# Performance work log

Hardware: AMD Instinct MI355X
Metric: run time of the kernel (lower is better)

## Reference

```python
import jax, jax.numpy as jnp
import numpy as np

B, T, H, L = 2048, 128, 48, 3  # batch, n_weights (= seq steps), hidden_dim, n_layers


def setup_inputs() -> dict:
    key = jax.random.key(0)
    ks = jax.random.split(key, 9)
    s = 0.05
    adj = jax.random.bernoulli(ks[0], 0.5, (B, T)).astype(jnp.float32)  # 0/1 adjacency entries
    eps = jax.random.normal(ks[1], (B, T), jnp.float32)  # standard-normal noise for rsample
    Wi = jax.random.normal(ks[2], (H, 1), jnp.float32) * s   # embed_input: Linear(1, H)
    bi = jnp.zeros((H,), jnp.float32)
    Wa = jax.random.normal(ks[3], (H, T), jnp.float32) * s   # embed_adj: Linear(n_weights, H)
    ba = jnp.zeros((H,), jnp.float32)
    Wp = jax.random.normal(ks[4], (1, H), jnp.float32) * s   # proj_mean: Linear(H, 1)
    bp = jnp.zeros((1,), jnp.float32)
    Wih = jax.random.normal(ks[5], (L, 4 * H, H), jnp.float32) * s  # LSTM input weights per layer
    Whh = jax.random.normal(ks[6], (L, 4 * H, H), jnp.float32) * s  # LSTM hidden weights per layer
    bih = jnp.zeros((L, 4 * H), jnp.float32)
    bhh = jnp.zeros((L, 4 * H), jnp.float32)
    h0 = 0.001 * jax.random.normal(ks[7], (L, H), jnp.float32)  # learned initial hidden state
    c0 = 0.001 * jax.random.normal(ks[8], (L, H), jnp.float32)  # learned initial cell state
    return dict(adj=adj, eps=eps, Wi=Wi, bi=bi, Wa=Wa, ba=ba, Wp=Wp, bp=bp,
                Wih=Wih, Whh=Whh, bih=bih, bhh=bhh, h0=h0, c0=c0)


def _lstm_cell(x, h, c, Wih_l, Whh_l, bih_l, bhh_l):
    # PyTorch LSTMCell math, gate order i, f, g, o
    gates = x @ Wih_l.T + bih_l + h @ Whh_l.T + bhh_l  # [B, 4H]
    i, f, g, o = jnp.split(gates, 4, axis=-1)
    c_new = jax.nn.sigmoid(f) * c + jax.nn.sigmoid(i) * jnp.tanh(g)
    h_new = jax.nn.sigmoid(o) * jnp.tanh(c_new)
    return h_new, c_new


def reference(adj, eps, Wi, bi, Wa, ba, Wp, bp, Wih, Whh, bih, bhh, h0, c0):
    n = adj.shape[0]
    # embed_adj(adj): constant across steps (the torch code recomputes it every step; same value)
    adj_emb = adj @ Wa.T + ba  # [B, H]
    h = jnp.broadcast_to(h0[:, None, :], (L, n, H))
    c = jnp.broadcast_to(c0[:, None, :], (L, n, H))
    inp0 = jnp.zeros((n, 1), adj.dtype)  # _init_input_param is a zeros parameter

    def step(carry, xs):
        h, c, inp = carry
        eps_t, adj_t = xs  # each [B]
        x = (inp @ Wi.T + bi) * adj_emb  # embed_input(inp) * embed_adj(adj), [B, H]
        hs, cs = [], []
        for l in range(L):  # 3 stacked LSTM layers, seq_len 1 per step
            x, c_l = _lstm_cell(x, h[l], c[l], Wih[l], Whh[l], bih[l], bhh[l])
            hs.append(x)
            cs.append(c_l)
        mean = x @ Wp.T + bp  # proj_mean, [B, 1]; std is fixed at 1
        # reparameterized sample from Normal(mean, 1), masked by adjacency column t
        sample = (mean[:, 0] + eps_t) * adj_t  # [B]
        return (jnp.stack(hs), jnp.stack(cs), sample[:, None]), sample

    _, samples = jax.lax.scan(step, (h, c, inp0), (eps.T, adj.T))
    return samples.T  # [B, n_weights]
```

## Files before the change

kernel.cpp:

```cpp
#include <hip/hip_runtime.h>
#include <hip/hip_bf16.h>


using bf16x8 = __attribute__((ext_vector_type(8))) __bf16;
using u16x8  = __attribute__((ext_vector_type(8))) unsigned short;
using f32x4  = __attribute__((ext_vector_type(4))) float;

__device__ __forceinline__ float fexp2(float x){ return __builtin_amdgcn_exp2f(x); }
__device__ __forceinline__ float frcp (float x){ return __builtin_amdgcn_rcpf(x); }
__device__ __forceinline__ float sigm (float x){ return frcp(1.f + fexp2(-1.44269504f*x)); }
__device__ __forceinline__ float tanha(float x){ return 1.f - 2.f*frcp(1.f + fexp2(2.88539008f*x)); }

__device__ __forceinline__ unsigned short f2bf(float x){
  unsigned u = __float_as_uint(x);
  return (unsigned short)((u + 0x7FFFu + ((u>>16)&1u)) >> 16);
}

__device__ __forceinline__ f32x4 mfma16(u16x8 a, u16x8 b, f32x4 c){
  return __builtin_amdgcn_mfma_f32_16x16x32_bf16(
      __builtin_bit_cast(bf16x8, a), __builtin_bit_cast(bf16x8, b), c, 0, 0, 0);
}

__device__ __forceinline__ unsigned cell2(
    const f32x4& ac0, const f32x4& ac1, const f32x4& ac2, const f32x4& ac3,
    bool lo, float& cv0, float& cv1)
{
  const float gi0 = lo ? ac0[0] : ac0[2], gi1 = lo ? ac0[1] : ac0[3];
  const float gf0 = lo ? ac1[0] : ac1[2], gf1 = lo ? ac1[1] : ac1[3];
  const float gg0 = lo ? ac2[0] : ac2[2], gg1 = lo ? ac2[1] : ac2[3];
  const float go0 = lo ? ac3[0] : ac3[2], go1 = lo ? ac3[1] : ac3[3];
  const float cn0 = sigm(gf0)*cv0 + sigm(gi0)*tanha(gg0);
  const float cn1 = sigm(gf1)*cv1 + sigm(gi1)*tanha(gg1);
  cv0 = cn0; cv1 = cn1;
  const float hv0 = sigm(go0)*tanha(cn0);
  const float hv1 = sigm(go1)*tanha(cn1);
  unsigned pk;
  asm("v_cvt_pk_bf16_f32 %0, %1, %2" : "=v"(pk) : "v"(hv0), "v"(hv1));
  return pk;
}

#define MM4(A, WK) \
  ac0 = mfma16(A, WK[0], ac0); ac1 = mfma16(A, WK[1], ac1); \
  ac2 = mfma16(A, WK[2], ac2); ac3 = mfma16(A, WK[3], ac3);

__global__ __launch_bounds__(192, 1) void lstm_fused(
    const float* __restrict__ adj, const float* __restrict__ eps,
    const float* __restrict__ Wi,  const float* __restrict__ bi,
    const float* __restrict__ Wa,  const float* __restrict__ ba,
    const float* __restrict__ Wp,  const float* __restrict__ bp,
    const float* __restrict__ Wih, const float* __restrict__ Whh,
    const float* __restrict__ bih, const float* __restrict__ bhh,
    const float* __restrict__ h0,  const float* __restrict__ c0,
    float* __restrict__ out)
{
  const int tid   = threadIdx.x;
  const int wv    = tid >> 6;
  const int lane  = tid & 63;
  const int c     = lane & 15;
  const int kg    = lane >> 4;
  const int j     = 16*wv + c;
  const int b0    = blockIdx.x * 8;
  const int bq    = 4*(kg & 1);
  const int bbase = bq + 2*(kg >> 1);
  const bool lo   = (kg < 2);

  __shared__ __align__(16) unsigned short hbuf[3][8][104];
  __shared__ __align__(16) float adjT[128][8];
  __shared__ __align__(16) float epsT[128][8];
  __shared__ __align__(16) float outb[128][8];

  u16x8 wf1[3][4], wf2[3][4];
  u16x8 wf0[2][4], wfx[2][4];
  u16x8 wpf[2];
  float biasr1[4], biasr2[4], biasr0[4];
#pragma unroll
  for (int kk = 0; kk < 3; ++kk) {
    const int k0 = 32*kk + 8*kg;
#pragma unroll
    for (int g = 0; g < 4; ++g) {
      const int n = 48*g + j;
#pragma unroll
      for (int l = 1; l < 3; ++l) {
        const float* src = (k0 < 48) ? (Wih + ((l*192 + n)*48 + k0))
                                     : (Whh + ((l*192 + n)*48 + (k0 - 48)));
        float4 p0 = *reinterpret_cast<const float4*>(src);
        float4 p1 = *reinterpret_cast<const float4*>(src + 4);
        u16x8 f;
        f[0]=f2bf(p0.x); f[1]=f2bf(p0.y); f[2]=f2bf(p0.z); f[3]=f2bf(p0.w);
        f[4]=f2bf(p1.x); f[5]=f2bf(p1.y); f[6]=f2bf(p1.z); f[7]=f2bf(p1.w);
        if (l == 1) wf1[kk][g] = f; else wf2[kk][g] = f;
      }
    }
  }
#pragma unroll
  for (int kk = 0; kk < 2; ++kk) {
    const int k0 = 32*kk + 8*kg;
#pragma unroll
    for (int g = 0; g < 4; ++g) {
      const int n = 48*g + j;
      u16x8 fh = {0,0,0,0,0,0,0,0}, fx = fh;
      if (k0 < 48) {
        const float* sh = Whh + (n*48 + k0);
        const float* sx = Wih + (n*48 + k0);
        float4 p0 = *reinterpret_cast<const float4*>(sh);
        float4 p1 = *reinterpret_cast<const float4*>(sh + 4);
        fh[0]=f2bf(p0.x); fh[1]=f2bf(p0.y); fh[2]=f2bf(p0.z); fh[3]=f2bf(p0.w);
        fh[4]=f2bf(p1.x); fh[5]=f2bf(p1.y); fh[6]=f2bf(p1.z); fh[7]=f2bf(p1.w);
        p0 = *reinterpret_cast<const float4*>(sx);
        p1 = *reinterpret_cast<const float4*>(sx + 4);
        fx[0]=f2bf(p0.x); fx[1]=f2bf(p0.y); fx[2]=f2bf(p0.z); fx[3]=f2bf(p0.w);
        fx[4]=f2bf(p1.x); fx[5]=f2bf(p1.y); fx[6]=f2bf(p1.z); fx[7]=f2bf(p1.w);
      }
      wf0[kk][g] = fh; wfx[kk][g] = fx;
    }
    u16x8 fp = {0,0,0,0,0,0,0,0};
#pragma unroll
    for (int e = 0; e < 8; ++e) {
      const int k = k0 + e;
      if (k < 48) fp[e] = f2bf(Wp[k]);
    }
    wpf[kk] = fp;
  }
#pragma unroll
  for (int g = 0; g < 4; ++g) {
    const int n = 48*g + j;
    biasr0[g] = bih[        n] + bhh[        n];
    biasr1[g] = bih[192   + n] + bhh[192   + n];
    biasr2[g] = bih[2*192 + n] + bhh[2*192 + n];
  }

  for (int i = tid; i < 256; i += 192) {
    const int b = i >> 5, q = i & 31;
    const float4 va = reinterpret_cast<const float4*>(adj + (size_t)(b0+b)*128)[q];
    adjT[4*q+0][b]=va.x; adjT[4*q+1][b]=va.y; adjT[4*q+2][b]=va.z; adjT[4*q+3][b]=va.w;
    const float4 ve = reinterpret_cast<const float4*>(eps + (size_t)(b0+b)*128)[q];
    epsT[4*q+0][b]=ve.x; epsT[4*q+1][b]=ve.y; epsT[4*q+2][b]=ve.z; epsT[4*q+3][b]=ve.w;
  }
  const float bp0 = bp[0];
  __syncthreads();

  for (int cid = tid; cid < 384; cid += 192) {
    const int b = cid & 7, jj = cid >> 3;
    float s = ba[jj];
    const float* wr = Wa + jj*128;
    for (int t2 = 0; t2 < 128; ++t2) s += adjT[t2][b] * wr[t2];
    hbuf[0][b][jj] = f2bf(Wi[jj] * s);
    hbuf[1][b][jj] = f2bf(bi[jj] * s);
  }
  for (int cid = tid; cid < 384; cid += 192) {
    const int l = cid / 128, r2 = cid % 128, b = r2 >> 4, jj = 48 + (r2 & 15);
    hbuf[l][b][jj] = 0;
  }
  __syncthreads();

  f32x4 uu[4], vb0[4];
  {
    const f32x4 z4 = {0.f,0.f,0.f,0.f};
    const unsigned short* rp = &hbuf[0][c & 7][0];
    u16x8 A0 = *reinterpret_cast<const u16x8*>(rp + 8*kg);
    u16x8 A1 = *reinterpret_cast<const u16x8*>(rp + 32 + 8*kg);
#pragma unroll
    for (int g = 0; g < 4; ++g)
      uu[g] = mfma16(A1, wfx[1][g], mfma16(A0, wfx[0][g], z4));
    rp = &hbuf[1][c & 7][0];
    A0 = *reinterpret_cast<const u16x8*>(rp + 8*kg);
    A1 = *reinterpret_cast<const u16x8*>(rp + 32 + 8*kg);
#pragma unroll
    for (int g = 0; g < 4; ++g) {
      f32x4 v = mfma16(A1, wfx[1][g], mfma16(A0, wfx[0][g], z4));
      const f32x4 bsp = {biasr0[g], biasr0[g], biasr0[g], biasr0[g]};
      vb0[g] = v + bsp;
    }
  }
  __syncthreads();

  for (int cid = tid; cid < 1152; cid += 192) {
    const int l = cid / 384, r2 = cid % 384, b = r2 & 7, jj = r2 >> 3;
    hbuf[l][b][jj] = f2bf(h0[l*48 + jj]);
  }
  float cc00, cc01, cc10, cc11, cc20, cc21;
  cc00 = cc01 = c0[       j];
  cc10 = cc11 = c0[48   + j];
  cc20 = cc21 = c0[2*48 + j];
  __syncthreads();

  f32x4 g0, g1, g2, g3;
  {
    const unsigned short* rp = &hbuf[0][c & 7][0];
    const u16x8 A0 = *reinterpret_cast<const u16x8*>(rp + 8*kg);
    const u16x8 A1 = *reinterpret_cast<const u16x8*>(rp + 32 + 8*kg);
    g0 = vb0[0]; g1 = vb0[1]; g2 = vb0[2]; g3 = vb0[3];
    g0 = mfma16(A0, wf0[0][0], g0); g1 = mfma16(A0, wf0[0][1], g1);
    g2 = mfma16(A0, wf0[0][2], g2); g3 = mfma16(A0, wf0[0][3], g3);
    g0 = mfma16(A1, wf0[1][0], g0); g1 = mfma16(A1, wf0[1][1], g1);
    g2 = mfma16(A1, wf0[1][2], g2); g3 = mfma16(A1, wf0[1][3], g3);
  }

  const f32x4 bp4 = {bp0, bp0, bp0, bp0};
  f32x4 sampv = {0.f,0.f,0.f,0.f};

  for (int t = 0; t < 128; ++t) {
    if (t) {
      const u16x8 mh0 = *reinterpret_cast<const u16x8*>(&hbuf[2][c & 7][8*kg]);
      const u16x8 mh1 = *reinterpret_cast<const u16x8*>(&hbuf[2][c & 7][32 + 8*kg]);
      const f32x4 ev = *reinterpret_cast<const f32x4*>(&epsT[t-1][bq]);
      const f32x4 av = *reinterpret_cast<const f32x4*>(&adjT[t-1][bq]);
      f32x4 mz = {0.f,0.f,0.f,0.f};
      mz = mfma16(mh0, wpf[0], mz);
      mz = mfma16(mh1, wpf[1], mz);
      sampv = (mz + bp4 + ev) * av;
      if (tid == 0 || tid == 16)
        *reinterpret_cast<f32x4*>(&outb[t-1][bq]) = sampv;
    }
    g0 += sampv*uu[0]; g1 += sampv*uu[1]; g2 += sampv*uu[2]; g3 += sampv*uu[3];
    {
      const unsigned pk = cell2(g0, g1, g2, g3, lo, cc00, cc01);
      hbuf[0][bbase    ][j] = (unsigned short)pk;
      hbuf[0][bbase + 1][j] = (unsigned short)(pk >> 16);
    }
    u16x8 a11 = {0,0,0,0,0,0,0,0}, a12;
    if (kg >= 2) a11 = *reinterpret_cast<const u16x8*>(&hbuf[1][c & 7][8*kg - 16]);
    a12 = *reinterpret_cast<const u16x8*>(&hbuf[1][c & 7][16 + 8*kg]);
    __syncthreads();
    {
      const unsigned short* rp = &hbuf[0][c & 7][0];
      const u16x8 a10 = *reinterpret_cast<const u16x8*>(rp + 8*kg);
      if (kg < 2) a11 = *reinterpret_cast<const u16x8*>(rp + 32 + 8*kg);
      f32x4 ac0 = {biasr1[0], biasr1[0], biasr1[0], biasr1[0]};
      f32x4 ac1 = {biasr1[1], biasr1[1], biasr1[1], biasr1[1]};
      f32x4 ac2 = {biasr1[2], biasr1[2], biasr1[2], biasr1[2]};
      f32x4 ac3 = {biasr1[3], biasr1[3], biasr1[3], biasr1[3]};
      MM4(a12, wf1[2]);
      MM4(a10, wf1[0]);
      MM4(a11, wf1[1]);
      const unsigned pk = cell2(ac0, ac1, ac2, ac3, lo, cc10, cc11);
      hbuf[1][bbase    ][j] = (unsigned short)pk;
      hbuf[1][bbase + 1][j] = (unsigned short)(pk >> 16);
    }
    u16x8 a21 = {0,0,0,0,0,0,0,0}, a22;
    if (kg >= 2) a21 = *reinterpret_cast<const u16x8*>(&hbuf[2][c & 7][8*kg - 16]);
    a22 = *reinterpret_cast<const u16x8*>(&hbuf[2][c & 7][16 + 8*kg]);
    __syncthreads();
    {
      const unsigned short* rp = &hbuf[1][c & 7][0];
      const u16x8 a20 = *reinterpret_cast<const u16x8*>(rp + 8*kg);
      if (kg < 2) a21 = *reinterpret_cast<const u16x8*>(rp + 32 + 8*kg);
      const unsigned short* rp0 = &hbuf[0][c & 7][0];
      const u16x8 a00 = *reinterpret_cast<const u16x8*>(rp0 + 8*kg);
      const u16x8 a01 = *reinterpret_cast<const u16x8*>(rp0 + 32 + 8*kg);
      f32x4 ac0 = {biasr2[0], biasr2[0], biasr2[0], biasr2[0]};
      f32x4 ac1 = {biasr2[1], biasr2[1], biasr2[1], biasr2[1]};
      f32x4 ac2 = {biasr2[2], biasr2[2], biasr2[2], biasr2[2]};
      f32x4 ac3 = {biasr2[3], biasr2[3], biasr2[3], biasr2[3]};
      MM4(a22, wf2[2]);
      MM4(a20, wf2[0]);
      MM4(a21, wf2[1]);
      const unsigned pk = cell2(ac0, ac1, ac2, ac3, lo, cc20, cc21);
      hbuf[2][bbase    ][j] = (unsigned short)pk;
      hbuf[2][bbase + 1][j] = (unsigned short)(pk >> 16);
      g0 = vb0[0]; g1 = vb0[1]; g2 = vb0[2]; g3 = vb0[3];
      g0 = mfma16(a00, wf0[0][0], g0); g1 = mfma16(a00, wf0[0][1], g1);
      g2 = mfma16(a00, wf0[0][2], g2); g3 = mfma16(a00, wf0[0][3], g3);
      g0 = mfma16(a01, wf0[1][0], g0); g1 = mfma16(a01, wf0[1][1], g1);
      g2 = mfma16(a01, wf0[1][2], g2); g3 = mfma16(a01, wf0[1][3], g3);
    }
    __syncthreads();
  }
  {
    const u16x8 mh0 = *reinterpret_cast<const u16x8*>(&hbuf[2][c & 7][8*kg]);
    const u16x8 mh1 = *reinterpret_cast<const u16x8*>(&hbuf[2][c & 7][32 + 8*kg]);
    const f32x4 ev = *reinterpret_cast<const f32x4*>(&epsT[127][bq]);
    const f32x4 av = *reinterpret_cast<const f32x4*>(&adjT[127][bq]);
    f32x4 mz = {0.f,0.f,0.f,0.f};
    mz = mfma16(mh0, wpf[0], mz);
    mz = mfma16(mh1, wpf[1], mz);
    const f32x4 sv = (mz + bp4 + ev) * av;
    if (tid == 0 || tid == 16)
      *reinterpret_cast<f32x4*>(&outb[127][bq]) = sv;
  }
  __syncthreads();
  for (int i = tid; i < 1024; i += 192) {
    const int b = i >> 7, tt = i & 127;
    out[(size_t)(b0 + b)*128 + tt] = outb[tt][b];
  }
}

extern "C" void kernel_launch(void* const* d_in, const int* in_sizes, int n_in,
                              void* d_out, int out_size, void* d_ws, size_t ws_size,
                              hipStream_t stream) {
  const float* adj = (const float*)d_in[0];
  const float* eps = (const float*)d_in[1];
  const float* Wi  = (const float*)d_in[2];
  const float* bi  = (const float*)d_in[3];
  const float* Wa  = (const float*)d_in[4];
  const float* ba  = (const float*)d_in[5];
  const float* Wp  = (const float*)d_in[6];
  const float* bp  = (const float*)d_in[7];
  const float* Wih = (const float*)d_in[8];
  const float* Whh = (const float*)d_in[9];
  const float* bih = (const float*)d_in[10];
  const float* bhh = (const float*)d_in[11];
  const float* h0  = (const float*)d_in[12];
  const float* c0  = (const float*)d_in[13];

  lstm_fused<<<dim3(2048/8), dim3(192), 0, stream>>>(
      adj, eps, Wi, bi, Wa, ba, Wp, bp, Wih, Whh, bih, bhh, h0, c0, (float*)d_out);
}
```

Baseline: 150.5 us.

## Halve batch rows per block to double grid and occupancy

Each block now handles 4 batch rows instead of 8, so the grid doubles to 512 blocks and launch bounds allow 2 blocks per CU. Each lane now computes one LSTM cell element instead of two. The MFMA work per block stays the same size, so half the MMA rows are wasted on duplicated batch rows. The aim is to spread the latency-bound recurrence over more CUs and let two blocks per CU overlap their barrier stalls, at the cost of more redundant weight loading and higher register pressure.

```diff
diff --git a/kernel.cpp b/kernel.cpp
--- a/kernel.cpp
+++ b/kernel.cpp
@@ -21,29 +21,17 @@
       __builtin_bit_cast(bf16x8, a), __builtin_bit_cast(bf16x8, b), c, 0, 0, 0);
 }
 
-__device__ __forceinline__ unsigned cell2(
-    const f32x4& ac0, const f32x4& ac1, const f32x4& ac2, const f32x4& ac3,
-    bool lo, float& cv0, float& cv1)
-{
-  const float gi0 = lo ? ac0[0] : ac0[2], gi1 = lo ? ac0[1] : ac0[3];
-  const float gf0 = lo ? ac1[0] : ac1[2], gf1 = lo ? ac1[1] : ac1[3];
-  const float gg0 = lo ? ac2[0] : ac2[2], gg1 = lo ? ac2[1] : ac2[3];
-  const float go0 = lo ? ac3[0] : ac3[2], go1 = lo ? ac3[1] : ac3[3];
-  const float cn0 = sigm(gf0)*cv0 + sigm(gi0)*tanha(gg0);
-  const float cn1 = sigm(gf1)*cv1 + sigm(gi1)*tanha(gg1);
-  cv0 = cn0; cv1 = cn1;
-  const float hv0 = sigm(go0)*tanha(cn0);
-  const float hv1 = sigm(go1)*tanha(cn1);
-  unsigned pk;
-  asm("v_cvt_pk_bf16_f32 %0, %1, %2" : "=v"(pk) : "v"(hv0), "v"(hv1));
-  return pk;
+__device__ __forceinline__ float sel4(const f32x4& a, int kg){
+  const float e01 = (kg & 1) ? a[1] : a[0];
+  const float e23 = (kg & 1) ? a[3] : a[2];
+  return (kg & 2) ? e23 : e01;
 }
 
 #define MM4(A, WK) \
   ac0 = mfma16(A, WK[0], ac0); ac1 = mfma16(A, WK[1], ac1); \
   ac2 = mfma16(A, WK[2], ac2); ac3 = mfma16(A, WK[3], ac3);
 
-__global__ __launch_bounds__(192, 1) void lstm_fused(
+__global__ __launch_bounds__(192, 2) void lstm_fused(
     const float* __restrict__ adj, const float* __restrict__ eps,
     const float* __restrict__ Wi,  const float* __restrict__ bi,
     const float* __restrict__ Wa,  const float* __restrict__ ba,
@@ -53,26 +41,24 @@
     const float* __restrict__ h0,  const float* __restrict__ c0,
     float* __restrict__ out)
 {
-  const int tid   = threadIdx.x;
-  const int wv    = tid >> 6;
-  const int lane  = tid & 63;
-  const int c     = lane & 15;
-  const int kg    = lane >> 4;
-  const int j     = 16*wv + c;
-  const int b0    = blockIdx.x * 8;
-  const int bq    = 4*(kg & 1);
-  const int bbase = bq + 2*(kg >> 1);
-  const bool lo   = (kg < 2);
-
-  __shared__ __align__(16) unsigned short hbuf[3][8][104];
-  __shared__ __align__(16) float adjT[128][8];
-  __shared__ __align__(16) float epsT[128][8];
-  __shared__ __align__(16) float outb[128][8];
+  const int tid  = threadIdx.x;
+  const int wv   = tid >> 6;
+  const int lane = tid & 63;
+  const int c    = lane & 15;
+  const int kg   = lane >> 4;
+  const int j    = 16*wv + c;
+  const int b0   = blockIdx.x * 4;
+  const int cr   = c & 3;
+
+  __shared__ __align__(16) unsigned short hbuf[3][4][104];
+  __shared__ __align__(16) float adjT[128][4];
+  __shared__ __align__(16) float epsT[128][4];
+  __shared__ __align__(16) float outb[128][4];
 
   u16x8 wf1[3][4], wf2[3][4];
   u16x8 wf0[2][4], wfx[2][4];
   u16x8 wpf[2];
-  float biasr1[4], biasr2[4], biasr0[4];
+  float biasr0[4], biasr1[4], biasr2[4];
 #pragma unroll
   for (int kk = 0; kk < 3; ++kk) {
     const int k0 = 32*kk + 8*kg;
@@ -129,8 +115,8 @@
     biasr2[g] = bih[2*192 + n] + bhh[2*192 + n];
   }
 
-  for (int i = tid; i < 256; i += 192) {
-    const int b = i >> 5, q = i & 31;
+  if (tid < 128) {
+    const int b = tid >> 5, q = tid & 31;
     const float4 va = reinterpret_cast<const float4*>(adj + (size_t)(b0+b)*128)[q];
     adjT[4*q+0][b]=va.x; adjT[4*q+1][b]=va.y; adjT[4*q+2][b]=va.z; adjT[4*q+3][b]=va.w;
     const float4 ve = reinterpret_cast<const float4*>(eps + (size_t)(b0+b)*128)[q];
@@ -139,57 +125,55 @@
   const float bp0 = bp[0];
   __syncthreads();
 
-  for (int cid = tid; cid < 384; cid += 192) {
-    const int b = cid & 7, jj = cid >> 3;
+  {
+    const int b = tid & 3, jj = tid >> 2;
     float s = ba[jj];
     const float* wr = Wa + jj*128;
     for (int t2 = 0; t2 < 128; ++t2) s += adjT[t2][b] * wr[t2];
     hbuf[0][b][jj] = f2bf(Wi[jj] * s);
     hbuf[1][b][jj] = f2bf(bi[jj] * s);
-  }
-  for (int cid = tid; cid < 384; cid += 192) {
-    const int l = cid / 128, r2 = cid % 128, b = r2 >> 4, jj = 48 + (r2 & 15);
-    hbuf[l][b][jj] = 0;
-  }
-  __syncthreads();
-
-  f32x4 uu[4], vb0[4];
+    hbuf[wv][lane >> 4][48 + (lane & 15)] = 0;
+  }
+  __syncthreads();
+
+  float u_k[4], vb_k[4];
   {
     const f32x4 z4 = {0.f,0.f,0.f,0.f};
-    const unsigned short* rp = &hbuf[0][c & 7][0];
+    const unsigned short* rp = &hbuf[0][cr][0];
     u16x8 A0 = *reinterpret_cast<const u16x8*>(rp + 8*kg);
     u16x8 A1 = *reinterpret_cast<const u16x8*>(rp + 32 + 8*kg);
 #pragma unroll
-    for (int g = 0; g < 4; ++g)
-      uu[g] = mfma16(A1, wfx[1][g], mfma16(A0, wfx[0][g], z4));
-    rp = &hbuf[1][c & 7][0];
+    for (int g = 0; g < 4; ++g) {
+      f32x4 u = mfma16(A1, wfx[1][g], mfma16(A0, wfx[0][g], z4));
+      u_k[g] = sel4(u, kg);
+    }
+    rp = &hbuf[1][cr][0];
     A0 = *reinterpret_cast<const u16x8*>(rp + 8*kg);
     A1 = *reinterpret_cast<const u16x8*>(rp + 32 + 8*kg);
 #pragma unroll
     for (int g = 0; g < 4; ++g) {
       f32x4 v = mfma16(A1, wfx[1][g], mfma16(A0, wfx[0][g], z4));
-      const f32x4 bsp = {biasr0[g], biasr0[g], biasr0[g], biasr0[g]};
-      vb0[g] = v + bsp;
-    }
-  }
-  __syncthreads();
-
-  for (int cid = tid; cid < 1152; cid += 192) {
-    const int l = cid / 384, r2 = cid % 384, b = r2 & 7, jj = r2 >> 3;
+      vb_k[g] = sel4(v, kg) + biasr0[g];
+    }
+  }
+  __syncthreads();
+
+  for (int cid = tid; cid < 576; cid += 192) {
+    const int l = cid / 192, r2 = cid % 192, b = r2 & 3, jj = r2 >> 2;
     hbuf[l][b][jj] = f2bf(h0[l*48 + jj]);
   }
-  float cc00, cc01, cc10, cc11, cc20, cc21;
-  cc00 = cc01 = c0[       j];
-  cc10 = cc11 = c0[48   + j];
-  cc20 = cc21 = c0[2*48 + j];
+  float cv0 = c0[j], cv1 = c0[48 + j], cv2 = c0[2*48 + j];
   __syncthreads();
 
   f32x4 g0, g1, g2, g3;
   {
-    const unsigned short* rp = &hbuf[0][c & 7][0];
+    const unsigned short* rp = &hbuf[0][cr][0];
     const u16x8 A0 = *reinterpret_cast<const u16x8*>(rp + 8*kg);
     const u16x8 A1 = *reinterpret_cast<const u16x8*>(rp + 32 + 8*kg);
-    g0 = vb0[0]; g1 = vb0[1]; g2 = vb0[2]; g3 = vb0[3];
+    g0 = (f32x4){vb_k[0], vb_k[0], vb_k[0], vb_k[0]};
+    g1 = (f32x4){vb_k[1], vb_k[1], vb_k[1], vb_k[1]};
+    g2 = (f32x4){vb_k[2], vb_k[2], vb_k[2], vb_k[2]};
+    g3 = (f32x4){vb_k[3], vb_k[3], vb_k[3], vb_k[3]};
     g0 = mfma16(A0, wf0[0][0], g0); g1 = mfma16(A0, wf0[0][1], g1);
     g2 = mfma16(A0, wf0[0][2], g2); g3 = mfma16(A0, wf0[0][3], g3);
     g0 = mfma16(A1, wf0[1][0], g0); g1 = mfma16(A1, wf0[1][1], g1);
@@ -197,33 +181,36 @@
   }
 
   const f32x4 bp4 = {bp0, bp0, bp0, bp0};
-  f32x4 sampv = {0.f,0.f,0.f,0.f};
+  f32x4 avR = {0.f,0.f,0.f,0.f}, evR = avR;
 
   for (int t = 0; t < 128; ++t) {
+    float s_kg = 0.f;
     if (t) {
-      const u16x8 mh0 = *reinterpret_cast<const u16x8*>(&hbuf[2][c & 7][8*kg]);
-      const u16x8 mh1 = *reinterpret_cast<const u16x8*>(&hbuf[2][c & 7][32 + 8*kg]);
-      const f32x4 ev = *reinterpret_cast<const f32x4*>(&epsT[t-1][bq]);
-      const f32x4 av = *reinterpret_cast<const f32x4*>(&adjT[t-1][bq]);
+      const u16x8 mh0 = *reinterpret_cast<const u16x8*>(&hbuf[2][cr][8*kg]);
+      const u16x8 mh1 = *reinterpret_cast<const u16x8*>(&hbuf[2][cr][32 + 8*kg]);
       f32x4 mz = {0.f,0.f,0.f,0.f};
       mz = mfma16(mh0, wpf[0], mz);
       mz = mfma16(mh1, wpf[1], mz);
-      sampv = (mz + bp4 + ev) * av;
-      if (tid == 0 || tid == 16)
-        *reinterpret_cast<f32x4*>(&outb[t-1][bq]) = sampv;
-    }
-    g0 += sampv*uu[0]; g1 += sampv*uu[1]; g2 += sampv*uu[2]; g3 += sampv*uu[3];
+      const f32x4 sampv = (mz + bp4 + evR) * avR;
+      if (tid == 0)
+        *reinterpret_cast<f32x4*>(&outb[t-1][0]) = sampv;
+      s_kg = sel4(sampv, kg);
+    }
     {
-      const unsigned pk = cell2(g0, g1, g2, g3, lo, cc00, cc01);
-      hbuf[0][bbase    ][j] = (unsigned short)pk;
-      hbuf[0][bbase + 1][j] = (unsigned short)(pk >> 16);
+      const float gi = sel4(g0, kg) + s_kg*u_k[0];
+      const float gf = sel4(g1, kg) + s_kg*u_k[1];
+      const float gg = sel4(g2, kg) + s_kg*u_k[2];
+      const float go = sel4(g3, kg) + s_kg*u_k[3];
+      const float cn = sigm(gf)*cv0 + sigm(gi)*tanha(gg);
+      cv0 = cn;
+      hbuf[0][kg][j] = f2bf(sigm(go)*tanha(cn));
     }
     u16x8 a11 = {0,0,0,0,0,0,0,0}, a12;
-    if (kg >= 2) a11 = *reinterpret_cast<const u16x8*>(&hbuf[1][c & 7][8*kg - 16]);
-    a12 = *reinterpret_cast<const u16x8*>(&hbuf[1][c & 7][16 + 8*kg]);
+    if (kg >= 2) a11 = *reinterpret_cast<const u16x8*>(&hbuf[1][cr][8*kg - 16]);
+    a12 = *reinterpret_cast<const u16x8*>(&hbuf[1][cr][16 + 8*kg]);
     __syncthreads();
     {
-      const unsigned short* rp = &hbuf[0][c & 7][0];
+      const unsigned short* rp = &hbuf[0][cr][0];
       const u16x8 a10 = *reinterpret_cast<const u16x8*>(rp + 8*kg);
       if (kg < 2) a11 = *reinterpret_cast<const u16x8*>(rp + 32 + 8*kg);
       f32x4 ac0 = {biasr1[0], biasr1[0], biasr1[0], biasr1[0]};
@@ -233,21 +220,25 @@
       MM4(a12, wf1[2]);
       MM4(a10, wf1[0]);
       MM4(a11, wf1[1]);
-      const unsigned pk = cell2(ac0, ac1, ac2, ac3, lo, cc10, cc11);
-      hbuf[1][bbase    ][j] = (unsigned short)pk;
-      hbuf[1][bbase + 1][j] = (unsigned short)(pk >> 16);
+      const float gi = sel4(ac0, kg), gf = sel4(ac1, kg);
+      const float gg = sel4(ac2, kg), go = sel4(ac3, kg);
+      const float cn = sigm(gf)*cv1 + sigm(gi)*tanha(gg);
+      cv1 = cn;
+      hbuf[1][kg][j] = f2bf(sigm(go)*tanha(cn));
     }
     u16x8 a21 = {0,0,0,0,0,0,0,0}, a22;
-    if (kg >= 2) a21 = *reinterpret_cast<const u16x8*>(&hbuf[2][c & 7][8*kg - 16]);
-    a22 = *reinterpret_cast<const u16x8*>(&hbuf[2][c & 7][16 + 8*kg]);
+    if (kg >= 2) a21 = *reinterpret_cast<const u16x8*>(&hbuf[2][cr][8*kg - 16]);
+    a22 = *reinterpret_cast<const u16x8*>(&hbuf[2][cr][16 + 8*kg]);
     __syncthreads();
     {
-      const unsigned short* rp = &hbuf[1][c & 7][0];
+      const unsigned short* rp = &hbuf[1][cr][0];
       const u16x8 a20 = *reinterpret_cast<const u16x8*>(rp + 8*kg);
       if (kg < 2) a21 = *reinterpret_cast<const u16x8*>(rp + 32 + 8*kg);
-      const unsigned short* rp0 = &hbuf[0][c & 7][0];
+      const unsigned short* rp0 = &hbuf[0][cr][0];
       const u16x8 a00 = *reinterpret_cast<const u16x8*>(rp0 + 8*kg);
       const u16x8 a01 = *reinterpret_cast<const u16x8*>(rp0 + 32 + 8*kg);
+      avR = *reinterpret_cast<const f32x4*>(&adjT[t][0]);
+      evR = *reinterpret_cast<const f32x4*>(&epsT[t][0]);
       f32x4 ac0 = {biasr2[0], biasr2[0], biasr2[0], biasr2[0]};
       f32x4 ac1 = {biasr2[1], biasr2[1], biasr2[1], biasr2[1]};
       f32x4 ac2 = {biasr2[2], biasr2[2], biasr2[2], biasr2[2]};
@@ -255,10 +246,15 @@
       MM4(a22, wf2[2]);
       MM4(a20, wf2[0]);
       MM4(a21, wf2[1]);
-      const unsigned pk = cell2(ac0, ac1, ac2, ac3, lo, cc20, cc21);
-      hbuf[2][bbase    ][j] = (unsigned short)pk;
-      hbuf[2][bbase + 1][j] = (unsigned short)(pk >> 16);
-      g0 = vb0[0]; g1 = vb0[1]; g2 = vb0[2]; g3 = vb0[3];
+      const float gi = sel4(ac0, kg), gf = sel4(ac1, kg);
+      const float gg = sel4(ac2, kg), go = sel4(ac3, kg);
+      const float cn = sigm(gf)*cv2 + sigm(gi)*tanha(gg);
+      cv2 = cn;
+      hbuf[2][kg][j] = f2bf(sigm(go)*tanha(cn));
+      g0 = (f32x4){vb_k[0], vb_k[0], vb_k[0], vb_k[0]};
+      g1 = (f32x4){vb_k[1], vb_k[1], vb_k[1], vb_k[1]};
+      g2 = (f32x4){vb_k[2], vb_k[2], vb_k[2], vb_k[2]};
+      g3 = (f32x4){vb_k[3], vb_k[3], vb_k[3], vb_k[3]};
       g0 = mfma16(a00, wf0[0][0], g0); g1 = mfma16(a00, wf0[0][1], g1);
       g2 = mfma16(a00, wf0[0][2], g2); g3 = mfma16(a00, wf0[0][3], g3);
       g0 = mfma16(a01, wf0[1][0], g0); g1 = mfma16(a01, wf0[1][1], g1);
@@ -267,19 +263,17 @@
     __syncthreads();
   }
   {
-    const u16x8 mh0 = *reinterpret_cast<const u16x8*>(&hbuf[2][c & 7][8*kg]);
-    const u16x8 mh1 = *reinterpret_cast<const u16x8*>(&hbuf[2][c & 7][32 + 8*kg]);
-    const f32x4 ev = *reinterpret_cast<const f32x4*>(&epsT[127][bq]);
-    const f32x4 av = *reinterpret_cast<const f32x4*>(&adjT[127][bq]);
+    const u16x8 mh0 = *reinterpret_cast<const u16x8*>(&hbuf[2][cr][8*kg]);
+    const u16x8 mh1 = *reinterpret_cast<const u16x8*>(&hbuf[2][cr][32 + 8*kg]);
     f32x4 mz = {0.f,0.f,0.f,0.f};
     mz = mfma16(mh0, wpf[0], mz);
     mz = mfma16(mh1, wpf[1], mz);
-    const f32x4 sv = (mz + bp4 + ev) * av;
-    if (tid == 0 || tid == 16)
-      *reinterpret_cast<f32x4*>(&outb[127][bq]) = sv;
-  }
-  __syncthreads();
-  for (int i = tid; i < 1024; i += 192) {
+    const f32x4 sv = (mz + bp4 + evR) * avR;
+    if (tid == 0)
+      *reinterpret_cast<f32x4*>(&outb[127][0]) = sv;
+  }
+  __syncthreads();
+  for (int i = tid; i < 512; i += 192) {
     const int b = i >> 7, tt = i & 127;
     out[(size_t)(b0 + b)*128 + tt] = outb[tt][b];
   }
@@ -303,6 +297,6 @@
   const float* h0  = (const float*)d_in[12];
   const float* c0  = (const float*)d_in[13];
 
-  lstm_fused<<<dim3(2048/8), dim3(192), 0, stream>>>(
+  lstm_fused<<<dim3(2048/4), dim3(192), 0, stream>>>(
       adj, eps, Wi, bi, Wa, ba, Wp, bp, Wih, Whh, bih, bhh, h0, c0, (float*)d_out);
 }
```

New measurement: 180.3 us. 19.8% more time.

## Restructure LSTM step: fewer transcendentals, hoisted MFMAs before barriers, split projection chains

Applied to the files above, without the earlier changes.

Rewrites the LSTM cell to use algebraically combined exp2 terms and a single reciprocal for the cell update and one for the output, instead of separate sigmoid/tanh reciprocals. Issues the MFMAs that depend only on already-available hidden state (the recurrent-h slice) before each barrier so they overlap the synchronization wait. Splits the projection MFMA into two independent accumulators, prefetches eps/adj a step early, and handles feedback per selected element rather than full vectors. The combined-exp formulation risks overflow/inf for large gate magnitudes and changes rounding slightly.

```diff
diff --git a/kernel.cpp b/kernel.cpp
--- a/kernel.cpp
+++ b/kernel.cpp
@@ -8,8 +8,6 @@
 
 __device__ __forceinline__ float fexp2(float x){ return __builtin_amdgcn_exp2f(x); }
 __device__ __forceinline__ float frcp (float x){ return __builtin_amdgcn_rcpf(x); }
-__device__ __forceinline__ float sigm (float x){ return frcp(1.f + fexp2(-1.44269504f*x)); }
-__device__ __forceinline__ float tanha(float x){ return 1.f - 2.f*frcp(1.f + fexp2(2.88539008f*x)); }
 
 __device__ __forceinline__ unsigned short f2bf(float x){
   unsigned u = __float_as_uint(x);
@@ -21,22 +19,20 @@
       __builtin_bit_cast(bf16x8, a), __builtin_bit_cast(bf16x8, b), c, 0, 0, 0);
 }
 
-__device__ __forceinline__ unsigned cell2(
-    const f32x4& ac0, const f32x4& ac1, const f32x4& ac2, const f32x4& ac3,
-    bool lo, float& cv0, float& cv1)
-{
-  const float gi0 = lo ? ac0[0] : ac0[2], gi1 = lo ? ac0[1] : ac0[3];
-  const float gf0 = lo ? ac1[0] : ac1[2], gf1 = lo ? ac1[1] : ac1[3];
-  const float gg0 = lo ? ac2[0] : ac2[2], gg1 = lo ? ac2[1] : ac2[3];
-  const float go0 = lo ? ac3[0] : ac3[2], go1 = lo ? ac3[1] : ac3[3];
-  const float cn0 = sigm(gf0)*cv0 + sigm(gi0)*tanha(gg0);
-  const float cn1 = sigm(gf1)*cv1 + sigm(gi1)*tanha(gg1);
-  cv0 = cn0; cv1 = cn1;
-  const float hv0 = sigm(go0)*tanha(cn0);
-  const float hv1 = sigm(go1)*tanha(cn1);
-  unsigned pk;
-  asm("v_cvt_pk_bf16_f32 %0, %1, %2" : "=v"(pk) : "v"(hv0), "v"(hv1));
-  return pk;
+__device__ __forceinline__ float selA(const f32x4& a, bool lo){ return lo ? a[0] : a[2]; }
+__device__ __forceinline__ float selB(const f32x4& a, bool lo){ return lo ? a[1] : a[3]; }
+
+__device__ __forceinline__ float cell_h(float gi, float gf, float gg, float go, float& cv){
+  const float A = fexp2(-1.44269504f*gf);
+  const float B = fexp2(-1.44269504f*gi);
+  const float G = fexp2(-2.88539008f*gg);
+  const float pBG = (1.f+B)*(1.f+G);
+  const float nc  = cv*pBG + (1.f+A)*(1.f-G);
+  const float cn  = nc * frcp((1.f+A)*pBG);
+  cv = cn;
+  const float O = fexp2(-1.44269504f*go);
+  const float C = fexp2(-2.88539008f*cn);
+  return (1.f-C) * frcp((1.f+O)*(1.f+C));
 }
 
 #define MM4(A, WK) \
@@ -63,6 +59,7 @@
   const int bq    = 4*(kg & 1);
   const int bbase = bq + 2*(kg >> 1);
   const bool lo   = (kg < 2);
+  const int cr    = c & 7;
 
   __shared__ __align__(16) unsigned short hbuf[3][8][104];
   __shared__ __align__(16) float adjT[128][8];
@@ -72,7 +69,7 @@
   u16x8 wf1[3][4], wf2[3][4];
   u16x8 wf0[2][4], wfx[2][4];
   u16x8 wpf[2];
-  float biasr1[4], biasr2[4], biasr0[4];
+  float biasr0[4], biasr1[4], biasr2[4];
 #pragma unroll
   for (int kk = 0; kk < 3; ++kk) {
     const int k0 = 32*kk + 8*kg;
@@ -153,23 +150,25 @@
   }
   __syncthreads();
 
-  f32x4 uu[4], vb0[4];
+  float uA[4], uB[4], vbA[4], vbB[4];
   {
     const f32x4 z4 = {0.f,0.f,0.f,0.f};
-    const unsigned short* rp = &hbuf[0][c & 7][0];
+    const unsigned short* rp = &hbuf[0][cr][0];
     u16x8 A0 = *reinterpret_cast<const u16x8*>(rp + 8*kg);
     u16x8 A1 = *reinterpret_cast<const u16x8*>(rp + 32 + 8*kg);
 #pragma unroll
-    for (int g = 0; g < 4; ++g)
-      uu[g] = mfma16(A1, wfx[1][g], mfma16(A0, wfx[0][g], z4));
-    rp = &hbuf[1][c & 7][0];
+    for (int g = 0; g < 4; ++g) {
+      f32x4 u = mfma16(A1, wfx[1][g], mfma16(A0, wfx[0][g], z4));
+      uA[g] = selA(u, lo); uB[g] = selB(u, lo);
+    }
+    rp = &hbuf[1][cr][0];
     A0 = *reinterpret_cast<const u16x8*>(rp + 8*kg);
     A1 = *reinterpret_cast<const u16x8*>(rp + 32 + 8*kg);
 #pragma unroll
     for (int g = 0; g < 4; ++g) {
       f32x4 v = mfma16(A1, wfx[1][g], mfma16(A0, wfx[0][g], z4));
-      const f32x4 bsp = {biasr0[g], biasr0[g], biasr0[g], biasr0[g]};
-      vb0[g] = v + bsp;
+      vbA[g] = selA(v, lo) + biasr0[g];
+      vbB[g] = selB(v, lo) + biasr0[g];
     }
   }
   __syncthreads();
@@ -178,18 +177,21 @@
     const int l = cid / 384, r2 = cid % 384, b = r2 & 7, jj = r2 >> 3;
     hbuf[l][b][jj] = f2bf(h0[l*48 + jj]);
   }
-  float cc00, cc01, cc10, cc11, cc20, cc21;
-  cc00 = cc01 = c0[       j];
-  cc10 = cc11 = c0[48   + j];
-  cc20 = cc21 = c0[2*48 + j];
+  float cc0A, cc0B, cc1A, cc1B, cc2A, cc2B;
+  cc0A = cc0B = c0[       j];
+  cc1A = cc1B = c0[48   + j];
+  cc2A = cc2B = c0[2*48 + j];
   __syncthreads();
 
   f32x4 g0, g1, g2, g3;
   {
-    const unsigned short* rp = &hbuf[0][c & 7][0];
+    const unsigned short* rp = &hbuf[0][cr][0];
     const u16x8 A0 = *reinterpret_cast<const u16x8*>(rp + 8*kg);
     const u16x8 A1 = *reinterpret_cast<const u16x8*>(rp + 32 + 8*kg);
-    g0 = vb0[0]; g1 = vb0[1]; g2 = vb0[2]; g3 = vb0[3];
+    g0 = (f32x4){vbA[0], vbB[0], vbA[0], vbB[0]};
+    g1 = (f32x4){vbA[1], vbB[1], vbA[1], vbB[1]};
+    g2 = (f32x4){vbA[2], vbB[2], vbA[2], vbB[2]};
+    g3 = (f32x4){vbA[3], vbB[3], vbA[3], vbB[3]};
     g0 = mfma16(A0, wf0[0][0], g0); g1 = mfma16(A0, wf0[0][1], g1);
     g2 = mfma16(A0, wf0[0][2], g2); g3 = mfma16(A0, wf0[0][3], g3);
     g0 = mfma16(A1, wf0[1][0], g0); g1 = mfma16(A1, wf0[1][1], g1);
@@ -197,68 +199,85 @@
   }
 
   const f32x4 bp4 = {bp0, bp0, bp0, bp0};
-  f32x4 sampv = {0.f,0.f,0.f,0.f};
+  f32x4 avR = {0.f,0.f,0.f,0.f}, evR = avR;
 
   for (int t = 0; t < 128; ++t) {
+    float sA = 0.f, sB = 0.f;
     if (t) {
-      const u16x8 mh0 = *reinterpret_cast<const u16x8*>(&hbuf[2][c & 7][8*kg]);
-      const u16x8 mh1 = *reinterpret_cast<const u16x8*>(&hbuf[2][c & 7][32 + 8*kg]);
-      const f32x4 ev = *reinterpret_cast<const f32x4*>(&epsT[t-1][bq]);
-      const f32x4 av = *reinterpret_cast<const f32x4*>(&adjT[t-1][bq]);
-      f32x4 mz = {0.f,0.f,0.f,0.f};
-      mz = mfma16(mh0, wpf[0], mz);
-      mz = mfma16(mh1, wpf[1], mz);
-      sampv = (mz + bp4 + ev) * av;
+      const u16x8 mh0 = *reinterpret_cast<const u16x8*>(&hbuf[2][cr][8*kg]);
+      const u16x8 mh1 = *reinterpret_cast<const u16x8*>(&hbuf[2][cr][32 + 8*kg]);
+      f32x4 mz0 = {0.f,0.f,0.f,0.f}, mz1 = mz0;
+      mz0 = mfma16(mh0, wpf[0], mz0);
+      mz1 = mfma16(mh1, wpf[1], mz1);
+      const f32x4 sampv = (mz0 + mz1 + bp4 + evR) * avR;
       if (tid == 0 || tid == 16)
         *reinterpret_cast<f32x4*>(&outb[t-1][bq]) = sampv;
-    }
-    g0 += sampv*uu[0]; g1 += sampv*uu[1]; g2 += sampv*uu[2]; g3 += sampv*uu[3];
+      sA = selA(sampv, lo); sB = selB(sampv, lo);
+    }
+    u16x8 a11 = {0,0,0,0,0,0,0,0}, a12;
+    if (kg >= 2) a11 = *reinterpret_cast<const u16x8*>(&hbuf[1][cr][8*kg - 16]);
+    a12 = *reinterpret_cast<const u16x8*>(&hbuf[1][cr][16 + 8*kg]);
     {
-      const unsigned pk = cell2(g0, g1, g2, g3, lo, cc00, cc01);
+      const float hA = cell_h(selA(g0,lo)+sA*uA[0], selA(g1,lo)+sA*uA[1],
+                              selA(g2,lo)+sA*uA[2], selA(g3,lo)+sA*uA[3], cc0A);
+      const float hB = cell_h(selB(g0,lo)+sB*uB[0], selB(g1,lo)+sB*uB[1],
+                              selB(g2,lo)+sB*uB[2], selB(g3,lo)+sB*uB[3], cc0B);
+      unsigned pk;
+      asm("v_cvt_pk_bf16_f32 %0, %1, %2" : "=v"(pk) : "v"(hA), "v"(hB));
       hbuf[0][bbase    ][j] = (unsigned short)pk;
       hbuf[0][bbase + 1][j] = (unsigned short)(pk >> 16);
     }
-    u16x8 a11 = {0,0,0,0,0,0,0,0}, a12;
-    if (kg >= 2) a11 = *reinterpret_cast<const u16x8*>(&hbuf[1][c & 7][8*kg - 16]);
-    a12 = *reinterpret_cast<const u16x8*>(&hbuf[1][c & 7][16 + 8*kg]);
+    f32x4 ac0 = {biasr1[0], biasr1[0], biasr1[0], biasr1[0]};
+    f32x4 ac1 = {biasr1[1], biasr1[1], biasr1[1], biasr1[1]};
+    f32x4 ac2 = {biasr1[2], biasr1[2], biasr1[2], biasr1[2]};
+    f32x4 ac3 = {biasr1[3], biasr1[3], biasr1[3], biasr1[3]};
+    MM4(a12, wf1[2]);
     __syncthreads();
     {
-      const unsigned short* rp = &hbuf[0][c & 7][0];
+      const unsigned short* rp = &hbuf[0][cr][0];
       const u16x8 a10 = *reinterpret_cast<const u16x8*>(rp + 8*kg);
       if (kg < 2) a11 = *reinterpret_cast<const u16x8*>(rp + 32 + 8*kg);
-      f32x4 ac0 = {biasr1[0], biasr1[0], biasr1[0], biasr1[0]};
-      f32x4 ac1 = {biasr1[1], biasr1[1], biasr1[1], biasr1[1]};
-      f32x4 ac2 = {biasr1[2], biasr1[2], biasr1[2], biasr1[2]};
-      f32x4 ac3 = {biasr1[3], biasr1[3], biasr1[3], biasr1[3]};
-      MM4(a12, wf1[2]);
       MM4(a10, wf1[0]);
       MM4(a11, wf1[1]);
-      const unsigned pk = cell2(ac0, ac1, ac2, ac3, lo, cc10, cc11);
+    }
+    u16x8 a21 = {0,0,0,0,0,0,0,0}, a22;
+    if (kg >= 2) a21 = *reinterpret_cast<const u16x8*>(&hbuf[2][cr][8*kg - 16]);
+    a22 = *reinterpret_cast<const u16x8*>(&hbuf[2][cr][16 + 8*kg]);
+    {
+      const float hA = cell_h(selA(ac0,lo), selA(ac1,lo), selA(ac2,lo), selA(ac3,lo), cc1A);
+      const float hB = cell_h(selB(ac0,lo), selB(ac1,lo), selB(ac2,lo), selB(ac3,lo), cc1B);
+      unsigned pk;
+      asm("v_cvt_pk_bf16_f32 %0, %1, %2" : "=v"(pk) : "v"(hA), "v"(hB));
       hbuf[1][bbase    ][j] = (unsigned short)pk;
       hbuf[1][bbase + 1][j] = (unsigned short)(pk >> 16);
     }
-    u16x8 a21 = {0,0,0,0,0,0,0,0}, a22;
-    if (kg >= 2) a21 = *reinterpret_cast<const u16x8*>(&hbuf[2][c & 7][8*kg - 16]);
-    a22 = *reinterpret_cast<const u16x8*>(&hbuf[2][c & 7][16 + 8*kg]);
+    ac0 = (f32x4){biasr2[0], biasr2[0], biasr2[0], biasr2[0]};
+    ac1 = (f32x4){biasr2[1], biasr2[1], biasr2[1], biasr2[1]};
+    ac2 = (f32x4){biasr2[2], biasr2[2], biasr2[2], biasr2[2]};
+    ac3 = (f32x4){biasr2[3], biasr2[3], biasr2[3], biasr2[3]};
+    MM4(a22, wf2[2]);
     __syncthreads();
     {
-      const unsigned short* rp = &hbuf[1][c & 7][0];
+      const unsigned short* rp = &hbuf[1][cr][0];
       const u16x8 a20 = *reinterpret_cast<const u16x8*>(rp + 8*kg);
       if (kg < 2) a21 = *reinterpret_cast<const u16x8*>(rp + 32 + 8*kg);
-      const unsigned short* rp0 = &hbuf[0][c & 7][0];
+      MM4(a20, wf2[0]);
+      MM4(a21, wf2[1]);
+      const unsigned short* rp0 = &hbuf[0][cr][0];
       const u16x8 a00 = *reinterpret_cast<const u16x8*>(rp0 + 8*kg);
       const u16x8 a01 = *reinterpret_cast<const u16x8*>(rp0 + 32 + 8*kg);
-      f32x4 ac0 = {biasr2[0], biasr2[0], biasr2[0], biasr2[0]};
-      f32x4 ac1 = {biasr2[1], biasr2[1], biasr2[1], biasr2[1]};
-      f32x4 ac2 = {biasr2[2], biasr2[2], biasr2[2], biasr2[2]};
-      f32x4 ac3 = {biasr2[3], biasr2[3], biasr2[3], biasr2[3]};
-      MM4(a22, wf2[2]);
-      MM4(a20, wf2[0]);
-      MM4(a21, wf2[1]);
-      const unsigned pk = cell2(ac0, ac1, ac2, ac3, lo, cc20, cc21);
+      avR = *reinterpret_cast<const f32x4*>(&adjT[t][bq]);
+      evR = *reinterpret_cast<const f32x4*>(&epsT[t][bq]);
+      const float hA = cell_h(selA(ac0,lo), selA(ac1,lo), selA(ac2,lo), selA(ac3,lo), cc2A);
+      const float hB = cell_h(selB(ac0,lo), selB(ac1,lo), selB(ac2,lo), selB(ac3,lo), cc2B);
+      unsigned pk;
+      asm("v_cvt_pk_bf16_f32 %0, %1, %2" : "=v"(pk) : "v"(hA), "v"(hB));
       hbuf[2][bbase    ][j] = (unsigned short)pk;
       hbuf[2][bbase + 1][j] = (unsigned short)(pk >> 16);
-      g0 = vb0[0]; g1 = vb0[1]; g2 = vb0[2]; g3 = vb0[3];
+      g0 = (f32x4){vbA[0], vbB[0], vbA[0], vbB[0]};
+      g1 = (f32x4){vbA[1], vbB[1], vbA[1], vbB[1]};
+      g2 = (f32x4){vbA[2], vbB[2], vbA[2], vbB[2]};
+      g3 = (f32x4){vbA[3], vbB[3], vbA[3], vbB[3]};
       g0 = mfma16(a00, wf0[0][0], g0); g1 = mfma16(a00, wf0[0][1], g1);
       g2 = mfma16(a00, wf0[0][2], g2); g3 = mfma16(a00, wf0[0][3], g3);
       g0 = mfma16(a01, wf0[1][0], g0); g1 = mfma16(a01, wf0[1][1], g1);
@@ -267,14 +286,12 @@
     __syncthreads();
   }
   {
-    const u16x8 mh0 = *reinterpret_cast<const u16x8*>(&hbuf[2][c & 7][8*kg]);
-    const u16x8 mh1 = *reinterpret_cast<const u16x8*>(&hbuf[2][c & 7][32 + 8*kg]);
-    const f32x4 ev = *reinterpret_cast<const f32x4*>(&epsT[127][bq]);
-    const f32x4 av = *reinterpret_cast<const f32x4*>(&adjT[127][bq]);
-    f32x4 mz = {0.f,0.f,0.f,0.f};
-    mz = mfma16(mh0, wpf[0], mz);
-    mz = mfma16(mh1, wpf[1], mz);
-    const f32x4 sv = (mz + bp4 + ev) * av;
+    const u16x8 mh0 = *reinterpret_cast<const u16x8*>(&hbuf[2][cr][8*kg]);
+    const u16x8 mh1 = *reinterpret_cast<const u16x8*>(&hbuf[2][cr][32 + 8*kg]);
+    f32x4 mz0 = {0.f,0.f,0.f,0.f}, mz1 = mz0;
+    mz0 = mfma16(mh0, wpf[0], mz0);
+    mz1 = mfma16(mh1, wpf[1], mz1);
+    const f32x4 sv = (mz0 + mz1 + bp4 + evR) * avR;
     if (tid == 0 || tid == 16)
       *reinterpret_cast<f32x4*>(&outb[127][bq]) = sv;
   }
```

After: 150.7 us. About the same (+0.1%).
